# Kernel optimization log

Hardware: AMD Instinct MI355X
Metric: run time of the kernel (lower is better)

The kernel has to match this reference:

```python
import jax, jax.numpy as jnp
import numpy as np

L, B, D, N = 4096, 8, 1024, 16


def setup_inputs() -> dict:
    key = jax.random.key(0)
    ks = jax.random.split(key, 6)
    # ema_expansion_matrix init: alternating +-1 plus small noise (per reset_parameters)
    sign = jnp.where(jnp.arange(N) % 2 == 1, -1.0, 1.0)[None, :, None]
    return {
        "x": jax.random.normal(ks[0], (L, B, D), dtype=jnp.float32),
        "damping_factor": 0.2 * jax.random.normal(ks[1], (D, N, 1), dtype=jnp.float32),
        "decay_factor": 0.2 * jax.random.normal(ks[2], (D, N, 1), dtype=jnp.float32),
        "ema_expansion_matrix": sign + 0.02 * jax.random.normal(ks[3], (D, N, 1), dtype=jnp.float32),
        "kernel_projection_matrix": jax.random.normal(ks[4], (D, N), dtype=jnp.float32),
        "residual_weight": jax.random.normal(ks[5], (D,), dtype=jnp.float32),
    }


def reference(x, damping_factor, decay_factor, ema_expansion_matrix,
              kernel_projection_matrix, residual_weight):
    # x: (L, B, D)
    length = x.shape[0]
    num_heads = damping_factor.shape[1]
    scaling = (1.0 / num_heads) ** 0.5

    residual = x * residual_weight  # (L, B, D)
    xc = jnp.transpose(x, (1, 2, 0))  # (B, D, L)

    # EMA coefficients
    p = jax.nn.sigmoid(damping_factor)                     # (D, N, 1)
    q = 1.0 - p * jax.nn.sigmoid(decay_factor)             # (D, N, 1)

    # Vandermonde kernel: (D, N, L) -> project to (D, L)
    t = jnp.arange(length, dtype=x.dtype)[None, None, :]
    kernel_dnl = p * ema_expansion_matrix * jnp.exp(t * jnp.log(q))
    kernel = jnp.einsum('dnl,dn->dl', kernel_dnl, kernel_projection_matrix * scaling)

    # Causal FFT convolution with n = 2L
    n_fft = 2 * length
    k_f = jnp.fft.rfft(kernel, n=n_fft)                    # (D, n/2+1)
    x_f = jnp.fft.rfft(xc, n=n_fft)                        # (B, D, n/2+1)
    out = jnp.fft.irfft(x_f * k_f, n=n_fft)[..., :length]  # (B, D, L)

    out = jnp.transpose(out, (2, 0, 1)) + residual         # (L, B, D)
    return jax.nn.relu(out)
```

## Files before the change

kernel.cpp:

```cpp
#include <hip/hip_runtime.h>
#include <math.h>

#define L 4096
#define B 8
#define D 1024
#define NH 16
#define COUT 128
#define WB 128
#define NCHUNK (L / COUT)
#define BD 8192
#define DBLK 128
#define TL 16

#define REP8(F)  F(0) F(1) F(2) F(3) F(4) F(5) F(6) F(7)

__device__ __forceinline__ float sigmoidf(float v) {
    return 1.0f / (1.0f + __expf(-v));
}

#define UPD(i) s##i = fmaf(q##i, s##i, xv);
#define UPDALL UPD(0) UPD(1) UPD(2) UPD(3) UPD(4) UPD(5) UPD(6) UPD(7)
#define ACC(i) s##i = fmaf(q##i, s##i, xv); y = fmaf(P##i, s##i, y);
#define ACCALL ACC(0) ACC(1) ACC(2) ACC(3) ACC(4) ACC(5) ACC(6) ACC(7)

#define GLD16(g, l) __builtin_amdgcn_global_load_lds( \
    (const __attribute__((address_space(1))) unsigned int*)(g), \
    (__attribute__((address_space(3))) unsigned int*)(l), 16, 0, 0)

__global__ void __launch_bounds__(256, 8)
ema_fused(const float* __restrict__ x,
          const float* __restrict__ damp,
          const float* __restrict__ decay,
          const float* __restrict__ ema,
          const float* __restrict__ proj,
          const float* __restrict__ rw,
          float* __restrict__ out) {
    const int tid  = threadIdx.x;
    const int lane = tid & 63;
    const int wv   = tid >> 6;
    const int h    = lane & 1;
    const int dloc = (wv << 5) + (lane >> 1);
    const int d0   = blockIdx.x * DBLK;
    const int d    = d0 + dloc;
    const int c    = blockIdx.y;
    const int b    = blockIdx.z;

    __shared__ float lds[2][TL * DBLK];

    const float* dp = damp  + d * NH + h * 8;
    const float* dc = decay + d * NH + h * 8;
    const float* de = ema   + d * NH + h * 8;
    const float* pj = proj  + d * NH + h * 8;

#define DECLQS(i) float q##i, s##i;
    REP8(DECLQS)
#define INITQS(i) { q##i = 1.0f - sigmoidf(dp[i]) * sigmoidf(dc[i]); s##i = 0.0f; }
    REP8(INITQS)
#define DECLP(i) float P##i;
    REP8(DECLP)
#define INITP(i) { float p_ = sigmoidf(dp[i]); P##i = p_ * de[i] * pj[i] * 0.25f; }
    REP8(INITP)
    const float weff = (h == 0) ? rw[d] : 0.0f;

    const int nt = (c > 0) ? (WB + COUT) / TL : COUT / TL;
    const int wt = (c > 0) ? WB / TL : 0;

    const float* xb = x + (size_t)(c * COUT - (c > 0 ? WB : 0)) * BD
                        + (size_t)b * D + d0;

    const int scol = (lane & 31) << 2;
    const int srow = (wv << 2) + (lane >> 5);

    {
        const float* g0 = xb + (size_t)srow * BD + scol;
        float* l0 = &lds[0][(wv << 2) * DBLK];
        GLD16(g0, l0);
        GLD16(g0 + (size_t)2 * BD, l0 + 2 * DBLK);
    }
    __syncthreads();

    float* opb = out + (size_t)(c * COUT) * BD + (size_t)b * D + d;

    for (int t = 0; t < nt; ++t) {
        if (t + 1 < nt) {
            const float* g0 = xb + (size_t)((t + 1) * TL + srow) * BD + scol;
            float* l0 = &lds[(t + 1) & 1][(wv << 2) * DBLK];
            GLD16(g0, l0);
            GLD16(g0 + (size_t)2 * BD, l0 + 2 * DBLK);
        }
        const float* buf = lds[t & 1];
        if (t < wt) {
#pragma unroll
            for (int sl = 0; sl < TL; ++sl) {
                float xv = buf[sl * DBLK + dloc];
                UPDALL
            }
        } else {
            float* op = opb + (size_t)(t - wt) * TL * BD;
#pragma unroll
            for (int sl = 0; sl < TL; ++sl) {
                float xv = buf[sl * DBLK + dloc];
                float y = xv * weff;
                ACCALL
                y += __shfl_xor(y, 1);
                if (h == 0)
                    __builtin_nontemporal_store(fmaxf(y, 0.0f), op + (size_t)sl * BD);
            }
        }
        __syncthreads();
    }
}

extern "C" void kernel_launch(void* const* d_in, const int* in_sizes, int n_in,
                              void* d_out, int out_size, void* d_ws, size_t ws_size,
                              hipStream_t stream) {
    const float* x     = (const float*)d_in[0];
    const float* damp  = (const float*)d_in[1];
    const float* decay = (const float*)d_in[2];
    const float* ema   = (const float*)d_in[3];
    const float* proj  = (const float*)d_in[4];
    const float* rw    = (const float*)d_in[5];
    float* out = (float*)d_out;

    dim3 grid(D / DBLK, NCHUNK, B);
    ema_fused<<<grid, 256, 0, stream>>>(x, damp, decay, ema, proj, rw, out);
}
```

Measured before the change: 283.2 us.

## Deepen LDS prefetch to four buffers with manual vmcnt waits and larger chunks

Replaces the double-buffered global-to-LDS prefetch with a four-buffer ring that keeps three tiles in flight. Synchronisation now uses explicit s_waitcnt vmcnt and a single raw barrier per tile instead of two __syncthreads. The output chunk grows from 128 to 256 steps, so the 128-step warm-up recurrence makes up a smaller share of each block's work. In exchange, the launch-bounds occupancy hint drops from 8 to 4 blocks, each block uses more LDS, and there are half as many blocks.

```diff
diff --git a/kernel.cpp b/kernel.cpp
--- a/kernel.cpp
+++ b/kernel.cpp
@@ -5,12 +5,13 @@
 #define B 8
 #define D 1024
 #define NH 16
-#define COUT 128
+#define COUT 256
 #define WB 128
 #define NCHUNK (L / COUT)
 #define BD 8192
 #define DBLK 128
 #define TL 16
+#define NBUF 4
 
 #define REP8(F)  F(0) F(1) F(2) F(3) F(4) F(5) F(6) F(7)
 
@@ -27,7 +28,10 @@
     (const __attribute__((address_space(1))) unsigned int*)(g), \
     (__attribute__((address_space(3))) unsigned int*)(l), 16, 0, 0)
 
-__global__ void __launch_bounds__(256, 8)
+#define VM(n) asm volatile("s_waitcnt vmcnt(" #n ")" ::: "memory")
+#define MEMFENCE asm volatile("" ::: "memory")
+
+__global__ void __launch_bounds__(256, 4)
 ema_fused(const float* __restrict__ x,
           const float* __restrict__ damp,
           const float* __restrict__ decay,
@@ -40,12 +44,11 @@
     const int wv   = tid >> 6;
     const int h    = lane & 1;
     const int dloc = (wv << 5) + (lane >> 1);
-    const int d0   = blockIdx.x * DBLK;
-    const int d    = d0 + dloc;
+    const int d    = blockIdx.x * DBLK + dloc;
     const int c    = blockIdx.y;
     const int b    = blockIdx.z;
 
-    __shared__ float lds[2][TL * DBLK];
+    __shared__ float lds[NBUF][TL * DBLK];
 
     const float* dp = damp  + d * NH + h * 8;
     const float* dc = decay + d * NH + h * 8;
@@ -62,52 +65,52 @@
     REP8(INITP)
     const float weff = (h == 0) ? rw[d] : 0.0f;
 
-    const int nt = (c > 0) ? (WB + COUT) / TL : COUT / TL;
-    const int wt = (c > 0) ? WB / TL : 0;
+    const int wb = (c > 0) ? WB : 0;
+    const int wt = wb / TL;
+    const int nt = wt + COUT / TL;
 
-    const float* xb = x + (size_t)(c * COUT - (c > 0 ? WB : 0)) * BD
-                        + (size_t)b * D + d0;
+    const float* xb = x + (size_t)(c * COUT - wb) * BD + (size_t)b * D
+                        + (size_t)blockIdx.x * DBLK;
+    const float* gsrc = xb + (size_t)((wv << 2) + (lane >> 5)) * BD
+                           + ((lane & 31) << 2);
 
-    const int scol = (lane & 31) << 2;
-    const int srow = (wv << 2) + (lane >> 5);
+#define GLD(t) { \
+        const float* g_ = gsrc + (size_t)(t) * (TL * BD); \
+        float* l_ = &lds[(t) & 3][(wv << 2) * DBLK]; \
+        GLD16(g_, l_); \
+        GLD16(g_ + 2 * (size_t)BD, l_ + 2 * DBLK); }
 
-    {
-        const float* g0 = xb + (size_t)srow * BD + scol;
-        float* l0 = &lds[0][(wv << 2) * DBLK];
-        GLD16(g0, l0);
-        GLD16(g0 + (size_t)2 * BD, l0 + 2 * DBLK);
-    }
-    __syncthreads();
+    GLD(0) GLD(1) GLD(2)
+    MEMFENCE;
 
     float* opb = out + (size_t)(c * COUT) * BD + (size_t)b * D + d;
 
     for (int t = 0; t < nt; ++t) {
-        if (t + 1 < nt) {
-            const float* g0 = xb + (size_t)((t + 1) * TL + srow) * BD + scol;
-            float* l0 = &lds[(t + 1) & 1][(wv << 2) * DBLK];
-            GLD16(g0, l0);
-            GLD16(g0 + (size_t)2 * BD, l0 + 2 * DBLK);
-        }
-        const float* buf = lds[t & 1];
+        if (t < nt - 2)       { VM(4); }
+        else if (t == nt - 2) { VM(2); }
+        else                  { VM(0); }
+        __builtin_amdgcn_s_barrier();
+        MEMFENCE;
+        if (t + 3 < nt) GLD(t + 3)
+        MEMFENCE;
+
+        const float* bp = &lds[t & 3][dloc];
         if (t < wt) {
 #pragma unroll
-            for (int sl = 0; sl < TL; ++sl) {
-                float xv = buf[sl * DBLK + dloc];
-                UPDALL
-            }
+            for (int sl = 0; sl < TL; ++sl) { float xv = bp[sl * DBLK]; UPDALL }
         } else {
-            float* op = opb + (size_t)(t - wt) * TL * BD;
+            float* op = opb + (size_t)(t - wt) * (TL * BD);
 #pragma unroll
             for (int sl = 0; sl < TL; ++sl) {
-                float xv = buf[sl * DBLK + dloc];
+                float xv = bp[sl * DBLK];
                 float y = xv * weff;
                 ACCALL
                 y += __shfl_xor(y, 1);
                 if (h == 0)
-                    __builtin_nontemporal_store(fmaxf(y, 0.0f), op + (size_t)sl * BD);
+                    __builtin_nontemporal_store(fmaxf(y, 0.0f),
+                                                op + (size_t)sl * BD);
             }
         }
-        __syncthreads();
     }
 }
 
```

After: 268.7 us. 5.1% less time.
